# Optimization experiments

Hardware: AMD Instinct MI355X
Metric: run time of the kernel (lower is better)

Reference implementation:

```python
import math
import jax
import jax.numpy as jnp
from jax import lax
import numpy as np

SEQ = 1024   # must be a perfect square
BSZ = 16
D = 1024     # embed_dim
NDIM = 2
SIDE = 32    # sqrt(SEQ) == one_side_length
SCALE = float(np.sqrt(1.0 / NDIM))


def setup_inputs() -> dict:
    key = jax.random.key(0)
    ks = jax.random.split(key, 8)
    x = jax.random.normal(ks[0], (SEQ, BSZ, D), dtype=jnp.float32)
    A1 = 0.2 * jax.random.normal(ks[1], (D, NDIM), dtype=jnp.float32)
    A2 = 0.2 * jax.random.normal(ks[2], (D, NDIM), dtype=jnp.float32)
    B1 = 0.2 * jax.random.normal(ks[3], (D, NDIM), dtype=jnp.float32)
    B2 = 0.2 * jax.random.normal(ks[4], (D, NDIM), dtype=jnp.float32)
    C1 = jax.random.normal(ks[5], (D, NDIM), dtype=jnp.float32)
    C2 = jax.random.normal(ks[6], (D, NDIM), dtype=jnp.float32)
    omega = jax.random.normal(ks[7], (D,), dtype=jnp.float32)
    return {"x": x, "A1": A1, "A2": A2, "B1": B1, "B2": B2,
            "C1": C1, "C2": C2, "omega": omega}


def _compute_kernel(A1, A2, B1, B2, C1, C2, n):
    """2D SSM impulse-response kernel K: (D, n, n).

    Recurrence (same math the coeff-matrix path-sum in compute_x_matrix encodes,
    cf. one_step):
      h[i,j] = a1*h[i,j-1] + a2*v[i,j-1] + b1*x[i,j]
      v[i,j] = a2*h[i-1,j] + a1*v[i-1,j] + b2*x[i,j]
      K[i,j] = <h[i,j], C1*scale> + <v[i,j], C2*scale>
    driven by a unit impulse at (0,0).
    """
    a1 = jax.nn.sigmoid(A1) * 0.5
    a2 = jax.nn.sigmoid(A2) * 0.5
    b1 = jax.nn.sigmoid(B1) * 0.5
    b2 = jax.nn.sigmoid(B2) * 0.5

    x_img = jnp.zeros((n, n), dtype=A1.dtype).at[0, 0].set(1.0)

    def row_step(carry, x_row):
        h_prev, v_prev = carry                     # (n, D, N) each
        v_row = a2 * h_prev + a1 * v_prev + b2 * x_row[:, None, None]
        # h depends on v of the PREVIOUS column in the current row
        sv = jnp.concatenate([jnp.zeros_like(v_row[:1]), v_row[:-1]], axis=0)

        def col_step(h_left, inp):
            sv_j, x_j = inp
            h_j = a1 * h_left + a2 * sv_j + b1 * x_j
            return h_j, h_j

        _, h_row = lax.scan(col_step, jnp.zeros((D, NDIM), dtype=A1.dtype),
                            (sv, x_row))
        return (h_row, v_row), (h_row, v_row)

    init = (jnp.zeros((n, D, NDIM), dtype=A1.dtype),
            jnp.zeros((n, D, NDIM), dtype=A1.dtype))
    _, (H, V) = lax.scan(row_step, init, x_img)    # (n, n, D, N)

    K = (jnp.einsum('ijdn,dn->ijd', H, C1 * SCALE)
         + jnp.einsum('ijdn,dn->ijd', V, C2 * SCALE))
    return jnp.transpose(K, (2, 0, 1))             # (D, n, n)


def reference(x, A1, A2, B1, B2, C1, C2, omega):
    seq_len, bsz, embed_dim = x.shape
    n = int(math.isqrt(seq_len))
    residual = x * omega                            # (S, B, D)

    k = _compute_kernel(A1, A2, B1, B2, C1, C2, n)  # (D, n, n)

    xi = jnp.transpose(x, (1, 2, 0)).reshape(bsz, embed_dim, n, n)
    s = (2 * n, 2 * n)
    kf = jnp.fft.rfft2(k.astype(jnp.float32), s=s)           # (D, 2n, n+1)
    xf = jnp.fft.rfft2(xi.astype(jnp.float32), s=s)          # (B, D, 2n, n+1)
    out = jnp.fft.irfft2(xf * kf, s=s)[..., :n, :n]          # (B, D, n, n)
    out = out.astype(x.dtype).reshape(bsz, embed_dim, seq_len)
    out = jnp.transpose(out, (2, 0, 1))                      # (S, B, D)
    return jax.nn.silu(out + residual)
```

## Files before the change

### kernel.cpp

```cpp
#include <hip/hip_runtime.h>
#include <math.h>

#define BSZ  16
#define DIM  1024
#define DPB  16
#define THREADS 1024
#define TPB  4
#define SSTRIDE 17
#define BUFF 17472
#define LDSB (2 * BUFF * 4)

__device__ __forceinline__ float sigmoidf_(float v) {
    return __builtin_amdgcn_rcpf(1.0f + __expf(-v));
}

extern __shared__ float xs[];

__global__ __launch_bounds__(THREADS, 1) void ssm2d_kernel(
    const float* __restrict__ x,
    const float* __restrict__ A1, const float* __restrict__ A2,
    const float* __restrict__ B1, const float* __restrict__ B2,
    const float* __restrict__ C1, const float* __restrict__ C2,
    const float* __restrict__ omega,
    float* __restrict__ out)
{
    const int bx = blockIdx.x;
    const int bq = bx >> 6;
    const int d0 = (bx & 63) * DPB;
    const int t  = threadIdx.x;

    const int lane = t & 63;
    const int wv   = t >> 6;
    const int i    = lane & 31;

    float a1c0, a1c1, a2c0, a2c1, b1c0, b1c1, b2c0, b2c1;
    float c1s0, c1s1, c2s0, c2s1, om;
    float a1z0, a1z1, a2z0, a2z1;
    int dd = 0;
    if (t < 512) {
        dd = 2 * wv + (lane >> 5);
        const int d = d0 + dd;
        const float2 fA1 = *reinterpret_cast<const float2*>(A1 + 2 * d);
        const float2 fA2 = *reinterpret_cast<const float2*>(A2 + 2 * d);
        const float2 fB1 = *reinterpret_cast<const float2*>(B1 + 2 * d);
        const float2 fB2 = *reinterpret_cast<const float2*>(B2 + 2 * d);
        const float2 fC1 = *reinterpret_cast<const float2*>(C1 + 2 * d);
        const float2 fC2 = *reinterpret_cast<const float2*>(C2 + 2 * d);
        om   = omega[d];
        a1c0 = sigmoidf_(fA1.x) * 0.5f;  a1c1 = sigmoidf_(fA1.y) * 0.5f;
        a2c0 = sigmoidf_(fA2.x) * 0.5f;  a2c1 = sigmoidf_(fA2.y) * 0.5f;
        b1c0 = sigmoidf_(fB1.x) * 0.5f;  b1c1 = sigmoidf_(fB1.y) * 0.5f;
        b2c0 = sigmoidf_(fB2.x) * 0.5f;  b2c1 = sigmoidf_(fB2.y) * 0.5f;
        const float sc = 0.70710678118654752f;
        c1s0 = fC1.x * sc;  c1s1 = fC1.y * sc;
        c2s0 = fC2.x * sc;  c2s1 = fC2.y * sc;
        a1z0 = (i == 0) ? 0.f : a1c0;  a1z1 = (i == 0) ? 0.f : a1c1;
        a2z0 = (i == 0) ? 0.f : a2c0;  a2z1 = (i == 0) ? 0.f : a2c1;
    }

    {
        const int   srow  = t >> 2;
        const int   qq    = (t & 3) * 4;
        const float* gp = x + (size_t)srow * (BSZ * DIM)
                            + (size_t)(4 * bq) * DIM + d0 + qq;
        float4 P[4];
        #pragma unroll
        for (int k2 = 0; k2 < 4; ++k2)
            P[k2] = *reinterpret_cast<const float4*>(
                gp + (size_t)k2 * (256 * BSZ * DIM));
        #pragma unroll
        for (int k2 = 0; k2 < 4; ++k2) {
            float* p = xs + SSTRIDE * (srow + 256 * k2) + qq;
            p[0] = P[k2].x; p[1] = P[k2].y; p[2] = P[k2].z; p[3] = P[k2].w;
        }
    }
    __syncthreads();

#define SSTEP(TS, XQ) do {                                                   \
        const bool  valid = ((unsigned)((TS) - i) < 32u);                    \
        const float xv    = valid ? (XQ) : 0.f;                              \
        const float t10 = b1c0 * xv, t11 = b1c1 * xv;                        \
        const float hn0 = fmaf(a1c0, h0, fmaf(a2c0, v0, t10));               \
        const float hn1 = fmaf(a1c1, h1, fmaf(a2c1, v1, t11));               \
        float vn0 = b2c0 * xv, vn1 = b2c1 * xv;                              \
        asm("s_nop 1\n\t"                                                    \
            "v_fmac_f32_dpp %0, %2, %6 wave_shr:1 row_mask:0xf bank_mask:0xf bound_ctrl:0\n\t" \
            "v_fmac_f32_dpp %1, %3, %7 wave_shr:1 row_mask:0xf bank_mask:0xf bound_ctrl:0\n\t" \
            "v_fmac_f32_dpp %0, %4, %8 wave_shr:1 row_mask:0xf bank_mask:0xf bound_ctrl:0\n\t" \
            "v_fmac_f32_dpp %1, %5, %9 wave_shr:1 row_mask:0xf bank_mask:0xf bound_ctrl:0"     \
            : "+v"(vn0), "+v"(vn1)                                           \
            : "v"(h0), "v"(h1), "v"(v0), "v"(v1),                            \
              "v"(a2z0), "v"(a2z1), "v"(a1z0), "v"(a1z1));                   \
        float y = hn0 * c1s0;                                                \
        y = fmaf(hn1, c1s1, y);                                              \
        y = fmaf(vn0, c2s0, y);                                              \
        y = fmaf(vn1, c2s1, y);                                              \
        const float z = fmaf(xv, om, y);                                     \
        const float o = z * sigmoidf_(z);                                    \
        if (valid) rp[SSTRIDE * (TS)] = o;                                   \
        h0 = hn0; h1 = hn1; v0 = vn0; v1 = vn1;                              \
    } while (0)

    #pragma unroll 1
    for (int k = 0; k < TPB; ++k) {
        float* bufC = xs + (k & 1) * BUFF;
        float* bufO = xs + ((k + 1) & 1) * BUFF;

        if (t < 512) {
            float* rp = bufC + 527 * i + dd;
            float h0 = 0.f, h1 = 0.f, v0 = 0.f, v1 = 0.f;
            float xq0 = rp[0 * SSTRIDE];
            float xq1 = rp[1 * SSTRIDE];
            float xq2 = rp[2 * SSTRIDE];
            #pragma unroll
            for (int ts = 0; ts < 63; ts += 3) {
                SSTEP(ts + 0, xq0); xq0 = rp[SSTRIDE * (ts + 3)];
                SSTEP(ts + 1, xq1); xq1 = rp[SSTRIDE * (ts + 4)];
                SSTEP(ts + 2, xq2); xq2 = rp[SSTRIDE * (ts + 5)];
            }
        } else {
            const int   m    = t - 512;
            const int   srow = m >> 2;
            const int   qq   = (m & 3) * 4;
            const size_t gb  = (size_t)srow * (BSZ * DIM) + d0 + qq;

            float4 L[8];
            if (k < TPB - 1) {
                const float* gp = x + gb + (size_t)(4 * bq + k + 1) * DIM;
                #pragma unroll
                for (int k2 = 0; k2 < 8; ++k2)
                    L[k2] = *reinterpret_cast<const float4*>(
                        gp + (size_t)k2 * (128 * BSZ * DIM));
            }
            if (k > 0) {
                float* op = out + gb + (size_t)(4 * bq + k - 1) * DIM;
                #pragma unroll
                for (int k2 = 0; k2 < 8; ++k2) {
                    const float* p = bufO + SSTRIDE * (srow + 128 * k2) + qq;
                    float4 v; v.x = p[0]; v.y = p[1]; v.z = p[2]; v.w = p[3];
                    *reinterpret_cast<float4*>(
                        op + (size_t)k2 * (128 * BSZ * DIM)) = v;
                }
            }
            if (k < TPB - 1) {
                #pragma unroll
                for (int k2 = 0; k2 < 8; ++k2) {
                    float* p = bufO + SSTRIDE * (srow + 128 * k2) + qq;
                    p[0] = L[k2].x; p[1] = L[k2].y;
                    p[2] = L[k2].z; p[3] = L[k2].w;
                }
            }
        }
        __syncthreads();
    }
#undef SSTEP

    {
        const int   srow = t >> 2;
        const int   qq   = (t & 3) * 4;
        const float* bufE = xs + ((TPB - 1) & 1) * BUFF;
        float* op = out + (size_t)srow * (BSZ * DIM)
                        + (size_t)(4 * bq + TPB - 1) * DIM + d0 + qq;
        #pragma unroll
        for (int k2 = 0; k2 < 4; ++k2) {
            const float* p = bufE + SSTRIDE * (srow + 256 * k2) + qq;
            float4 v; v.x = p[0]; v.y = p[1]; v.z = p[2]; v.w = p[3];
            *reinterpret_cast<float4*>(op + (size_t)k2 * (256 * BSZ * DIM)) = v;
        }
    }
}

extern "C" void kernel_launch(void* const* d_in, const int* in_sizes, int n_in,
                              void* d_out, int out_size, void* d_ws, size_t ws_size,
                              hipStream_t stream) {
    const float* x     = (const float*)d_in[0];
    const float* A1    = (const float*)d_in[1];
    const float* A2    = (const float*)d_in[2];
    const float* B1    = (const float*)d_in[3];
    const float* B2    = (const float*)d_in[4];
    const float* C1    = (const float*)d_in[5];
    const float* C2    = (const float*)d_in[6];
    const float* omega = (const float*)d_in[7];
    float* out = (float*)d_out;

    (void)hipFuncSetAttribute(reinterpret_cast<const void*>(ssm2d_kernel),
                              hipFuncAttributeMaxDynamicSharedMemorySize, LDSB);

    dim3 grid(256);
    dim3 block(THREADS);
    hipLaunchKernelGGL(ssm2d_kernel, grid, block, LDSB, stream,
                       x, A1, A2, B1, B2, C1, C2, omega, out);
}
```

Baseline: 40.58 us.

## Prefetch future x tiles earlier, split scan validity checks, raise loader priority

The loader half-block now issues the global loads for tile 1 during the prologue, and for tiles 2 and 3 one iteration ahead, holding them in registers. This hides global-load latency behind compute instead of waiting within the same iteration. The diagonal scan loop is split into a pre-diagonal part and a post-diagonal part, each with a simpler validity check, which removes the per-step masking of the input on the post half. The loader waves raise their scheduling priority with s_setprio while issuing memory work. The cost is higher register pressure from 24 float4 prefetch buffers.

```diff
diff --git a/kernel.cpp b/kernel.cpp
--- a/kernel.cpp
+++ b/kernel.cpp
@@ -58,27 +58,56 @@
         a2z0 = (i == 0) ? 0.f : a2c0;  a2z1 = (i == 0) ? 0.f : a2c1;
     }
 
+    const int m    = t & 511;
+    const int srow = m >> 2;
+    const int qq   = (m & 3) * 4;
+    const size_t gb = (size_t)srow * (BSZ * DIM) + d0 + qq;
+    float4 LP[8], LA[8], LB[8];
+
+#define ISSUE(DST, TILE) do {                                                \
+        const float* gp = x + gb + (size_t)(TILE) * DIM;                     \
+        _Pragma("unroll") for (int k2 = 0; k2 < 8; ++k2)                     \
+            DST[k2] = *reinterpret_cast<const float4*>(                      \
+                gp + (size_t)k2 * (128 * BSZ * DIM));                        \
+    } while (0)
+
+#define STAGEFROM(SRC, BUFO) do {                                            \
+        _Pragma("unroll") for (int k2 = 0; k2 < 8; ++k2) {                   \
+            float* p = (BUFO) + SSTRIDE * (srow + 128 * k2) + qq;            \
+            p[0] = SRC[k2].x; p[1] = SRC[k2].y;                              \
+            p[2] = SRC[k2].z; p[3] = SRC[k2].w; }                            \
+    } while (0)
+
+#define DRAINTO(TILE, BUFO) do {                                             \
+        float* op = out + gb + (size_t)(TILE) * DIM;                         \
+        _Pragma("unroll") for (int k2 = 0; k2 < 8; ++k2) {                   \
+            const float* p = (BUFO) + SSTRIDE * (srow + 128 * k2) + qq;      \
+            float4 v; v.x = p[0]; v.y = p[1]; v.z = p[2]; v.w = p[3];        \
+            *reinterpret_cast<float4*>(                                      \
+                op + (size_t)k2 * (128 * BSZ * DIM)) = v; }                  \
+    } while (0)
+
     {
-        const int   srow  = t >> 2;
-        const int   qq    = (t & 3) * 4;
-        const float* gp = x + (size_t)srow * (BSZ * DIM)
-                            + (size_t)(4 * bq) * DIM + d0 + qq;
+        const int srow4 = t >> 2;
+        const int qq4   = (t & 3) * 4;
+        const float* gp0 = x + (size_t)srow4 * (BSZ * DIM)
+                             + (size_t)(4 * bq) * DIM + d0 + qq4;
         float4 P[4];
         #pragma unroll
         for (int k2 = 0; k2 < 4; ++k2)
             P[k2] = *reinterpret_cast<const float4*>(
-                gp + (size_t)k2 * (256 * BSZ * DIM));
+                gp0 + (size_t)k2 * (256 * BSZ * DIM));
+        if (t >= 512) ISSUE(LP, 4 * bq + 1);
         #pragma unroll
         for (int k2 = 0; k2 < 4; ++k2) {
-            float* p = xs + SSTRIDE * (srow + 256 * k2) + qq;
+            float* p = xs + SSTRIDE * (srow4 + 256 * k2) + qq4;
             p[0] = P[k2].x; p[1] = P[k2].y; p[2] = P[k2].z; p[3] = P[k2].w;
         }
     }
     __syncthreads();
 
-#define SSTEP(TS, XQ) do {                                                   \
-        const bool  valid = ((unsigned)((TS) - i) < 32u);                    \
-        const float xv    = valid ? (XQ) : 0.f;                              \
+#define SBODY(XV_EXPR)                                                       \
+        const float xv = (XV_EXPR);                                          \
         const float t10 = b1c0 * xv, t11 = b1c1 * xv;                        \
         const float hn0 = fmaf(a1c0, h0, fmaf(a2c0, v0, t10));               \
         const float hn1 = fmaf(a1c1, h1, fmaf(a2c1, v1, t11));               \
@@ -96,74 +125,64 @@
         y = fmaf(vn0, c2s0, y);                                              \
         y = fmaf(vn1, c2s1, y);                                              \
         const float z = fmaf(xv, om, y);                                     \
-        const float o = z * sigmoidf_(z);                                    \
-        if (valid) rp[SSTRIDE * (TS)] = o;                                   \
-        h0 = hn0; h1 = hn1; v0 = vn0; v1 = vn1;                              \
-    } while (0)
+        const float o = z * sigmoidf_(z);
+
+#define SSTEP_PRE(TS, XQ) do {                                               \
+        const bool val = (i <= (TS));                                        \
+        SBODY(val ? (XQ) : 0.f)                                              \
+        if (val) rp[SSTRIDE * (TS)] = o;                                     \
+        h0 = hn0; h1 = hn1; v0 = vn0; v1 = vn1; } while (0)
+
+#define SSTEP_POST(TS, XQ) do { SBODY(XQ)                                    \
+        if (i >= (TS) - 31) rp[SSTRIDE * (TS)] = o;                          \
+        h0 = hn0; h1 = hn1; v0 = vn0; v1 = vn1; } while (0)
 
     #pragma unroll 1
     for (int k = 0; k < TPB; ++k) {
-        float* bufC = xs + (k & 1) * BUFF;
-        float* bufO = xs + ((k + 1) & 1) * BUFF;
-
         if (t < 512) {
-            float* rp = bufC + 527 * i + dd;
+            float* rp = xs + (k & 1) * BUFF + 527 * i + dd;
             float h0 = 0.f, h1 = 0.f, v0 = 0.f, v1 = 0.f;
             float xq0 = rp[0 * SSTRIDE];
             float xq1 = rp[1 * SSTRIDE];
             float xq2 = rp[2 * SSTRIDE];
             #pragma unroll
-            for (int ts = 0; ts < 63; ts += 3) {
-                SSTEP(ts + 0, xq0); xq0 = rp[SSTRIDE * (ts + 3)];
-                SSTEP(ts + 1, xq1); xq1 = rp[SSTRIDE * (ts + 4)];
-                SSTEP(ts + 2, xq2); xq2 = rp[SSTRIDE * (ts + 5)];
+            for (int ts = 0; ts < 30; ts += 3) {
+                SSTEP_PRE(ts + 0, xq0); xq0 = rp[SSTRIDE * (ts + 3)];
+                SSTEP_PRE(ts + 1, xq1); xq1 = rp[SSTRIDE * (ts + 4)];
+                SSTEP_PRE(ts + 2, xq2); xq2 = rp[SSTRIDE * (ts + 5)];
             }
+            SSTEP_PRE(30, xq0); xq0 = rp[SSTRIDE * 33];
+            #pragma unroll
+            for (int ts = 31; ts < 61; ts += 3) {
+                SSTEP_POST(ts + 0, xq1); xq1 = rp[SSTRIDE * (ts + 3)];
+                SSTEP_POST(ts + 1, xq2); xq2 = rp[SSTRIDE * (ts + 4)];
+                SSTEP_POST(ts + 2, xq0); xq0 = rp[SSTRIDE * (ts + 5)];
+            }
+            SSTEP_POST(61, xq1);
+            SSTEP_POST(62, xq2);
         } else {
-            const int   m    = t - 512;
-            const int   srow = m >> 2;
-            const int   qq   = (m & 3) * 4;
-            const size_t gb  = (size_t)srow * (BSZ * DIM) + d0 + qq;
-
-            float4 L[8];
-            if (k < TPB - 1) {
-                const float* gp = x + gb + (size_t)(4 * bq + k + 1) * DIM;
-                #pragma unroll
-                for (int k2 = 0; k2 < 8; ++k2)
-                    L[k2] = *reinterpret_cast<const float4*>(
-                        gp + (size_t)k2 * (128 * BSZ * DIM));
-            }
-            if (k > 0) {
-                float* op = out + gb + (size_t)(4 * bq + k - 1) * DIM;
-                #pragma unroll
-                for (int k2 = 0; k2 < 8; ++k2) {
-                    const float* p = bufO + SSTRIDE * (srow + 128 * k2) + qq;
-                    float4 v; v.x = p[0]; v.y = p[1]; v.z = p[2]; v.w = p[3];
-                    *reinterpret_cast<float4*>(
-                        op + (size_t)k2 * (128 * BSZ * DIM)) = v;
-                }
-            }
-            if (k < TPB - 1) {
-                #pragma unroll
-                for (int k2 = 0; k2 < 8; ++k2) {
-                    float* p = bufO + SSTRIDE * (srow + 128 * k2) + qq;
-                    p[0] = L[k2].x; p[1] = L[k2].y;
-                    p[2] = L[k2].z; p[3] = L[k2].w;
-                }
-            }
+            __builtin_amdgcn_s_setprio(1);
+            float* bufO = xs + ((k + 1) & 1) * BUFF;
+            if (k == 0) ISSUE(LA, 4 * bq + 2);
+            if (k == 1) ISSUE(LB, 4 * bq + 3);
+            if (k >= 1) DRAINTO(4 * bq + k - 1, bufO);
+            if (k == 0) STAGEFROM(LP, bufO);
+            if (k == 1) STAGEFROM(LA, bufO);
+            if (k == 2) STAGEFROM(LB, bufO);
+            __builtin_amdgcn_s_setprio(0);
         }
         __syncthreads();
     }
-#undef SSTEP
 
     {
-        const int   srow = t >> 2;
-        const int   qq   = (t & 3) * 4;
+        const int srow4 = t >> 2;
+        const int qq4   = (t & 3) * 4;
         const float* bufE = xs + ((TPB - 1) & 1) * BUFF;
-        float* op = out + (size_t)srow * (BSZ * DIM)
-                        + (size_t)(4 * bq + TPB - 1) * DIM + d0 + qq;
+        float* op = out + (size_t)srow4 * (BSZ * DIM)
+                        + (size_t)(4 * bq + TPB - 1) * DIM + d0 + qq4;
         #pragma unroll
         for (int k2 = 0; k2 < 4; ++k2) {
-            const float* p = bufE + SSTRIDE * (srow + 256 * k2) + qq;
+            const float* p = bufE + SSTRIDE * (srow4 + 256 * k2) + qq4;
             float4 v; v.x = p[0]; v.y = p[1]; v.z = p[2]; v.w = p[3];
             *reinterpret_cast<float4*>(op + (size_t)k2 * (256 * BSZ * DIM)) = v;
         }
```

New measurement: 56.17 us. 1.38x slower.
